# Kernel optimization log

Measured on AMD Instinct MI355X. Metric: run time of the kernel, lower is better.

## Reference

```python
import jax, jax.numpy as jnp
import numpy as np

# Dimensions (see shape_source)
N = 50000       # graph_size (number of nodes)
E_HALF = 300000 # undirected edges
E = 2 * E_HALF  # directed edges (both orientations)
D = 4           # stalk dimension d
H = 32          # hidden_channels


def _build_graph(seed=0):
    """Symmetric directed edge list: columns [0,E_HALF) are (u->v), columns
    [E_HALF, E) are the reversed (v->u). opp_idx[e] is the index of the
    opposite orientation of edge e (this is exactly the pairing computed by
    lap.compute_left_right_map_index in the torch module)."""
    rng = np.random.default_rng(seed)
    u = rng.integers(0, N, size=E_HALF)
    v = rng.integers(0, N, size=E_HALF)
    v = np.where(v == u, (v + 1) % N, v)  # no self-loops
    edge_index = np.stack([np.concatenate([u, v]), np.concatenate([v, u])]).astype(np.int32)
    opp = np.concatenate([np.arange(E_HALF) + E_HALF, np.arange(E_HALF)]).astype(np.int32)
    return jnp.asarray(edge_index), jnp.asarray(opp)


def setup_inputs() -> dict:
    key = jax.random.key(0)
    k1, k2, k3 = jax.random.split(key, 3)
    edge_index, opp_idx = _build_graph()
    x = jax.random.normal(k1, (N, D, H), dtype=jnp.float32)
    Maps = jax.random.normal(k2, (E, D, D), dtype=jnp.float32)
    # linear1: torch.nn.Linear(d*d, prod(out_shape)) with out_shape=(d,d)
    W1 = jax.random.normal(k3, (D * D, D * D), dtype=jnp.float32) / np.sqrt(D * D)
    b1 = jnp.zeros((D * D,), dtype=jnp.float32)
    return {"x": x, "Maps": Maps, "W1": W1, "b1": b1,
            "edge_index": edge_index, "opp_idx": opp_idx}


def reference(x, Maps, W1, b1, edge_index, opp_idx):
    # The dual-graph (nodes = directed edges) sheaf Laplacian of the
    # GeneralLaplacianBuilder reduces to a closed per-edge block form:
    # every dual node has degree 1, so deg-normalisation (deg_normalised=True,
    # augmented=False) is the identity. For directed edge e = (s -> t) with
    # opposite edge e' = opp_idx[e]:
    #   diag block of dual node e           =  X_s X_s^T
    #   off-diag block between e and e'     = -X_s X_t^T
    # spmm(L, Maps^T-blocks) followed by the x2 and transpose in forward gives
    #   sims_e = 2 * ( M_e (X_s X_s^T) - M_{e'} (X_t X_s^T) )
    s, t = edge_index[0], edge_index[1]
    Xs = x[s]                                   # (E, D, H) gather
    Xt = x[t]                                   # (E, D, H) gather
    G_ss = jnp.einsum('edh,ekh->edk', Xs, Xs)   # (E, D, D)  X_s X_s^T
    G_ts = jnp.einsum('edh,ekh->edk', Xt, Xs)   # (E, D, D)  X_t X_s^T
    sims = 2.0 * (jnp.einsum('eij,ejk->eik', Maps, G_ss)
                  - jnp.einsum('eij,ejk->eik', Maps[opp_idx], G_ts))
    # linear1 (torch Linear: y = x W^T + b) + tanh activation
    flat = sims.reshape(E, D * D) @ W1.T + b1
    return jnp.tanh(flat).reshape(E, D, D)      # out_shape = (d, d)
```

## Files before the change

kernel.cpp:

```cpp
#include <hip/hip_runtime.h>

constexpr int TPB = 256;
constexpr int PAIRS_PER_BLOCK = 32;

__device__ __forceinline__ float fast_tanh(float v) {
    float ex = __expf(2.0f * v);
    return 1.0f - 2.0f * __builtin_amdgcn_rcpf(ex + 1.0f);
}

template <int CTRL>
__device__ __forceinline__ float dppadd(float x) {
    return x + __int_as_float(__builtin_amdgcn_update_dpp(
        0, __float_as_int(x), CTRL, 0xf, 0xf, true));
}

__device__ __forceinline__ float sum8(float x) {
    x = dppadd<0x128>(x);
    x = dppadd<0x39>(x);
    x = dppadd<0x4E>(x);
    return x;
}

__global__ __launch_bounds__(TPB) void sheaf_p8_kernel(
    const float* __restrict__ x,
    const float* __restrict__ Maps,
    const float* __restrict__ W1,
    const float* __restrict__ b1,
    const int*   __restrict__ edge_index,
    const int*   __restrict__ opp_idx,
    float*       __restrict__ out,
    int E, int EHALF)
{
    const int tid    = threadIdx.x;
    const int lane16 = tid & 15;
    const int row16  = tid >> 4;
    const int pinr   = (lane16 >> 2) & 1;
    const int slot   = (lane16 & 3) | (((lane16 >> 3) & 1) << 2);
    const int pair   = blockIdx.x * PAIRS_PER_BLOCK + row16 * 2 + pinr;
    if (pair >= EHALF) return;

    const int s  = edge_index[pair];
    const int t  = edge_index[E + pair];
    const int e2 = opp_idx[pair];

    const float* xu = x + (size_t)s * 128 + slot * 4;
    const float* xv = x + (size_t)t * 128 + slot * 4;
    float4 u[4], v[4];
    #pragma unroll
    for (int d = 0; d < 4; ++d) {
        u[d] = *(const float4*)(xu + d * 32);
        v[d] = *(const float4*)(xv + d * 32);
    }

    const int p0 = 2 * slot;
    float wA[16], wB[16];
    {
        const float4* WpA = (const float4*)(W1 + p0 * 16);
        const float4* WpB = (const float4*)(W1 + (p0 + 1) * 16);
        #pragma unroll
        for (int q4 = 0; q4 < 4; ++q4) {
            float4 a = WpA[q4], b = WpB[q4];
            wA[q4*4+0] = a.x; wA[q4*4+1] = a.y; wA[q4*4+2] = a.z; wA[q4*4+3] = a.w;
            wB[q4*4+0] = b.x; wB[q4*4+1] = b.y; wB[q4*4+2] = b.z; wB[q4*4+3] = b.w;
        }
    }
    const float2 bb = *(const float2*)(b1 + p0);

    const float4* M1p = (const float4*)(Maps + (size_t)pair * 16);
    const float4* M2p = (const float4*)(Maps + (size_t)e2   * 16);

    float d1a = 0.f, d1b = 0.f, d2a = 0.f, d2b = 0.f;
    #pragma unroll
    for (int i = 0; i < 4; ++i) {
        const float4 m1 = M1p[i];
        const float4 m2 = M2p[i];
        float4 zi;
        zi.x = m1.x * u[0].x;            zi.y = m1.x * u[0].y;
        zi.z = m1.x * u[0].z;            zi.w = m1.x * u[0].w;
        zi.x = fmaf(m1.y, u[1].x, zi.x); zi.y = fmaf(m1.y, u[1].y, zi.y);
        zi.z = fmaf(m1.y, u[1].z, zi.z); zi.w = fmaf(m1.y, u[1].w, zi.w);
        zi.x = fmaf(m1.z, u[2].x, zi.x); zi.y = fmaf(m1.z, u[2].y, zi.y);
        zi.z = fmaf(m1.z, u[2].z, zi.z); zi.w = fmaf(m1.z, u[2].w, zi.w);
        zi.x = fmaf(m1.w, u[3].x, zi.x); zi.y = fmaf(m1.w, u[3].y, zi.y);
        zi.z = fmaf(m1.w, u[3].z, zi.z); zi.w = fmaf(m1.w, u[3].w, zi.w);
        zi.x = fmaf(-m2.x, v[0].x, zi.x); zi.y = fmaf(-m2.x, v[0].y, zi.y);
        zi.z = fmaf(-m2.x, v[0].z, zi.z); zi.w = fmaf(-m2.x, v[0].w, zi.w);
        zi.x = fmaf(-m2.y, v[1].x, zi.x); zi.y = fmaf(-m2.y, v[1].y, zi.y);
        zi.z = fmaf(-m2.y, v[1].z, zi.z); zi.w = fmaf(-m2.y, v[1].w, zi.w);
        zi.x = fmaf(-m2.z, v[2].x, zi.x); zi.y = fmaf(-m2.z, v[2].y, zi.y);
        zi.z = fmaf(-m2.z, v[2].z, zi.z); zi.w = fmaf(-m2.z, v[2].w, zi.w);
        zi.x = fmaf(-m2.w, v[3].x, zi.x); zi.y = fmaf(-m2.w, v[3].y, zi.y);
        zi.z = fmaf(-m2.w, v[3].z, zi.z); zi.w = fmaf(-m2.w, v[3].w, zi.w);

        #pragma unroll
        for (int k = 0; k < 4; ++k) {
            float pa = zi.x * u[k].x;
            pa = fmaf(zi.y, u[k].y, pa);
            pa = fmaf(zi.z, u[k].z, pa);
            pa = fmaf(zi.w, u[k].w, pa);
            float pb = zi.x * v[k].x;
            pb = fmaf(zi.y, v[k].y, pb);
            pb = fmaf(zi.z, v[k].z, pb);
            pb = fmaf(zi.w, v[k].w, pb);
            const float r1 = sum8(pa);
            const float r2 = sum8(pb);
            const int q = i * 4 + k;
            d1a = fmaf(wA[q], r1, d1a);
            d1b = fmaf(wB[q], r1, d1b);
            d2a = fmaf(wA[q], r2, d2a);
            d2b = fmaf(wB[q], r2, d2b);
        }
    }

    const float o1a = fast_tanh(fmaf( 2.0f, d1a, bb.x));
    const float o1b = fast_tanh(fmaf( 2.0f, d1b, bb.y));
    const float o2a = fast_tanh(fmaf(-2.0f, d2a, bb.x));
    const float o2b = fast_tanh(fmaf(-2.0f, d2b, bb.y));

    *(float2*)(out + (size_t)pair * 16 + p0) = make_float2(o1a, o1b);
    *(float2*)(out + (size_t)e2   * 16 + p0) = make_float2(o2a, o2b);
}

extern "C" void kernel_launch(void* const* d_in, const int* in_sizes, int n_in,
                              void* d_out, int out_size, void* d_ws, size_t ws_size,
                              hipStream_t stream) {
    const float* x          = (const float*)d_in[0];
    const float* Maps       = (const float*)d_in[1];
    const float* W1         = (const float*)d_in[2];
    const float* b1         = (const float*)d_in[3];
    const int*   edge_index = (const int*)d_in[4];
    const int*   opp_idx    = (const int*)d_in[5];

    const int E     = in_sizes[5];
    const int EHALF = E / 2;

    const int blocks = (EHALF + PAIRS_PER_BLOCK - 1) / PAIRS_PER_BLOCK;
    sheaf_p8_kernel<<<blocks, TPB, 0, stream>>>(
        x, Maps, W1, b1, edge_index, opp_idx, (float*)d_out, E, EHALF);
}
```

Before: 65.52 us.

## Convert to persistent grid-stride kernel with software-pipelined double-buffered loads

Replaces the one-chunk-per-block launch with a persistent grid of at most 1024 blocks that loop over pair chunks. Each iteration prefetches indices two chunks ahead and x/Maps data one chunk ahead into register double buffers while the current chunk is computed, so gather latency overlaps compute. W1 and bias are loaded once per thread and reused. The extra register buffers may cut occupancy, and fewer resident blocks reduce hardware latency hiding.

```diff
diff --git a/kernel.cpp b/kernel.cpp
--- a/kernel.cpp
+++ b/kernel.cpp
@@ -1,7 +1,7 @@
 #include <hip/hip_runtime.h>
 
 constexpr int TPB = 256;
-constexpr int PAIRS_PER_BLOCK = 32;
+constexpr int PPB = 32;
 
 __device__ __forceinline__ float fast_tanh(float v) {
     float ex = __expf(2.0f * v);
@@ -21,7 +21,7 @@
     return x;
 }
 
-__global__ __launch_bounds__(TPB) void sheaf_p8_kernel(
+__global__ __launch_bounds__(TPB) void sheaf_pipe_kernel(
     const float* __restrict__ x,
     const float* __restrict__ Maps,
     const float* __restrict__ W1,
@@ -36,21 +36,7 @@
     const int row16  = tid >> 4;
     const int pinr   = (lane16 >> 2) & 1;
     const int slot   = (lane16 & 3) | (((lane16 >> 3) & 1) << 2);
-    const int pair   = blockIdx.x * PAIRS_PER_BLOCK + row16 * 2 + pinr;
-    if (pair >= EHALF) return;
-
-    const int s  = edge_index[pair];
-    const int t  = edge_index[E + pair];
-    const int e2 = opp_idx[pair];
-
-    const float* xu = x + (size_t)s * 128 + slot * 4;
-    const float* xv = x + (size_t)t * 128 + slot * 4;
-    float4 u[4], v[4];
-    #pragma unroll
-    for (int d = 0; d < 4; ++d) {
-        u[d] = *(const float4*)(xu + d * 32);
-        v[d] = *(const float4*)(xv + d * 32);
-    }
+    const int NC     = (EHALF + PPB - 1) / PPB;
 
     const int p0 = 2 * slot;
     float wA[16], wB[16];
@@ -66,59 +52,124 @@
     }
     const float2 bb = *(const float2*)(b1 + p0);
 
-    const float4* M1p = (const float4*)(Maps + (size_t)pair * 16);
-    const float4* M2p = (const float4*)(Maps + (size_t)e2   * 16);
+    auto pairOf = [&](int c) { return c * PPB + row16 * 2 + pinr; };
 
-    float d1a = 0.f, d1b = 0.f, d2a = 0.f, d2b = 0.f;
-    #pragma unroll
-    for (int i = 0; i < 4; ++i) {
-        const float4 m1 = M1p[i];
-        const float4 m2 = M2p[i];
-        float4 zi;
-        zi.x = m1.x * u[0].x;            zi.y = m1.x * u[0].y;
-        zi.z = m1.x * u[0].z;            zi.w = m1.x * u[0].w;
-        zi.x = fmaf(m1.y, u[1].x, zi.x); zi.y = fmaf(m1.y, u[1].y, zi.y);
-        zi.z = fmaf(m1.y, u[1].z, zi.z); zi.w = fmaf(m1.y, u[1].w, zi.w);
-        zi.x = fmaf(m1.z, u[2].x, zi.x); zi.y = fmaf(m1.z, u[2].y, zi.y);
-        zi.z = fmaf(m1.z, u[2].z, zi.z); zi.w = fmaf(m1.z, u[2].w, zi.w);
-        zi.x = fmaf(m1.w, u[3].x, zi.x); zi.y = fmaf(m1.w, u[3].y, zi.y);
-        zi.z = fmaf(m1.w, u[3].z, zi.z); zi.w = fmaf(m1.w, u[3].w, zi.w);
-        zi.x = fmaf(-m2.x, v[0].x, zi.x); zi.y = fmaf(-m2.x, v[0].y, zi.y);
-        zi.z = fmaf(-m2.x, v[0].z, zi.z); zi.w = fmaf(-m2.x, v[0].w, zi.w);
-        zi.x = fmaf(-m2.y, v[1].x, zi.x); zi.y = fmaf(-m2.y, v[1].y, zi.y);
-        zi.z = fmaf(-m2.y, v[1].z, zi.z); zi.w = fmaf(-m2.y, v[1].w, zi.w);
-        zi.x = fmaf(-m2.z, v[2].x, zi.x); zi.y = fmaf(-m2.z, v[2].y, zi.y);
-        zi.z = fmaf(-m2.z, v[2].z, zi.z); zi.w = fmaf(-m2.z, v[2].w, zi.w);
-        zi.x = fmaf(-m2.w, v[3].x, zi.x); zi.y = fmaf(-m2.w, v[3].y, zi.y);
-        zi.z = fmaf(-m2.w, v[3].z, zi.z); zi.w = fmaf(-m2.w, v[3].w, zi.w);
+    auto loadIdx = [&](int c, int& s, int& t, int& e2) {
+        int pr = pairOf(c);
+        int pc = pr < EHALF ? pr : EHALF - 1;
+        s  = edge_index[pc];
+        t  = edge_index[E + pc];
+        e2 = opp_idx[pc];
+    };
+    auto loadX = [&](int s, int t, float4 (&u)[4], float4 (&v)[4]) {
+        const float* xu = x + (size_t)s * 128 + slot * 4;
+        const float* xv = x + (size_t)t * 128 + slot * 4;
+        #pragma unroll
+        for (int d = 0; d < 4; ++d) {
+            u[d] = *(const float4*)(xu + d * 32);
+            v[d] = *(const float4*)(xv + d * 32);
+        }
+    };
+    auto loadMaps = [&](int c, int e2, float4 (&m1)[4], float4 (&m2)[4]) {
+        int pr = pairOf(c);
+        int pc = pr < EHALF ? pr : EHALF - 1;
+        const float4* M1p = (const float4*)(Maps + (size_t)pc * 16);
+        const float4* M2p = (const float4*)(Maps + (size_t)e2 * 16);
+        #pragma unroll
+        for (int i = 0; i < 4; ++i) { m1[i] = M1p[i]; m2[i] = M2p[i]; }
+    };
 
+    auto computeStore = [&](int c, int e2,
+                            const float4 (&u)[4], const float4 (&v)[4],
+                            const float4 (&m1)[4], const float4 (&m2)[4]) {
+        float d1a = 0.f, d1b = 0.f, d2a = 0.f, d2b = 0.f;
         #pragma unroll
-        for (int k = 0; k < 4; ++k) {
-            float pa = zi.x * u[k].x;
-            pa = fmaf(zi.y, u[k].y, pa);
-            pa = fmaf(zi.z, u[k].z, pa);
-            pa = fmaf(zi.w, u[k].w, pa);
-            float pb = zi.x * v[k].x;
-            pb = fmaf(zi.y, v[k].y, pb);
-            pb = fmaf(zi.z, v[k].z, pb);
-            pb = fmaf(zi.w, v[k].w, pb);
-            const float r1 = sum8(pa);
-            const float r2 = sum8(pb);
-            const int q = i * 4 + k;
-            d1a = fmaf(wA[q], r1, d1a);
-            d1b = fmaf(wB[q], r1, d1b);
-            d2a = fmaf(wA[q], r2, d2a);
-            d2b = fmaf(wB[q], r2, d2b);
+        for (int i = 0; i < 4; ++i) {
+            const float4 M1 = m1[i], M2 = m2[i];
+            float4 zi;
+            zi.x = M1.x * u[0].x;            zi.y = M1.x * u[0].y;
+            zi.z = M1.x * u[0].z;            zi.w = M1.x * u[0].w;
+            zi.x = fmaf(M1.y, u[1].x, zi.x); zi.y = fmaf(M1.y, u[1].y, zi.y);
+            zi.z = fmaf(M1.y, u[1].z, zi.z); zi.w = fmaf(M1.y, u[1].w, zi.w);
+            zi.x = fmaf(M1.z, u[2].x, zi.x); zi.y = fmaf(M1.z, u[2].y, zi.y);
+            zi.z = fmaf(M1.z, u[2].z, zi.z); zi.w = fmaf(M1.z, u[2].w, zi.w);
+            zi.x = fmaf(M1.w, u[3].x, zi.x); zi.y = fmaf(M1.w, u[3].y, zi.y);
+            zi.z = fmaf(M1.w, u[3].z, zi.z); zi.w = fmaf(M1.w, u[3].w, zi.w);
+            zi.x = fmaf(-M2.x, v[0].x, zi.x); zi.y = fmaf(-M2.x, v[0].y, zi.y);
+            zi.z = fmaf(-M2.x, v[0].z, zi.z); zi.w = fmaf(-M2.x, v[0].w, zi.w);
+            zi.x = fmaf(-M2.y, v[1].x, zi.x); zi.y = fmaf(-M2.y, v[1].y, zi.y);
+            zi.z = fmaf(-M2.y, v[1].z, zi.z); zi.w = fmaf(-M2.y, v[1].w, zi.w);
+            zi.x = fmaf(-M2.z, v[2].x, zi.x); zi.y = fmaf(-M2.z, v[2].y, zi.y);
+            zi.z = fmaf(-M2.z, v[2].z, zi.z); zi.w = fmaf(-M2.z, v[2].w, zi.w);
+            zi.x = fmaf(-M2.w, v[3].x, zi.x); zi.y = fmaf(-M2.w, v[3].y, zi.y);
+            zi.z = fmaf(-M2.w, v[3].z, zi.z); zi.w = fmaf(-M2.w, v[3].w, zi.w);
+
+            #pragma unroll
+            for (int k = 0; k < 4; ++k) {
+                float pa = zi.x * u[k].x;
+                pa = fmaf(zi.y, u[k].y, pa);
+                pa = fmaf(zi.z, u[k].z, pa);
+                pa = fmaf(zi.w, u[k].w, pa);
+                float pb = zi.x * v[k].x;
+                pb = fmaf(zi.y, v[k].y, pb);
+                pb = fmaf(zi.z, v[k].z, pb);
+                pb = fmaf(zi.w, v[k].w, pb);
+                const float r1 = sum8(pa);
+                const float r2 = sum8(pb);
+                const int q = i * 4 + k;
+                d1a = fmaf(wA[q], r1, d1a);
+                d1b = fmaf(wB[q], r1, d1b);
+                d2a = fmaf(wA[q], r2, d2a);
+                d2b = fmaf(wB[q], r2, d2b);
+            }
         }
+        const float o1a = fast_tanh(fmaf( 2.0f, d1a, bb.x));
+        const float o1b = fast_tanh(fmaf( 2.0f, d1b, bb.y));
+        const float o2a = fast_tanh(fmaf(-2.0f, d2a, bb.x));
+        const float o2b = fast_tanh(fmaf(-2.0f, d2b, bb.y));
+
+        const int pr = pairOf(c);
+        if (pr < EHALF) {
+            *(float2*)(out + (size_t)pr * 16 + p0) = make_float2(o1a, o1b);
+            *(float2*)(out + (size_t)e2 * 16 + p0) = make_float2(o2a, o2b);
+        }
+    };
+
+    const int G = gridDim.x;
+    int cC = blockIdx.x;
+    if (cC >= NC) return;
+
+    float4 u0[4], v0[4], m10[4], m20[4];
+    float4 u1[4], v1[4], m11[4], m21[4];
+    int s1 = 0, t1 = 0, e1 = 0;
+    int sp = 0, tp = 0, ep = 0;
+
+    int s0, t0, e0;
+    loadIdx(cC, s0, t0, e0);
+    loadX(s0, t0, u0, v0);
+    loadMaps(cC, e0, m10, m20);
+    int cL = cC + G;
+    if (cL < NC) loadIdx(cL, s1, t1, e1);
+
+    for (;;) {
+        int cP = cL + G;
+        if (cL < NC) { loadX(s1, t1, u1, v1); loadMaps(cL, e1, m11, m21); }
+        if (cP < NC) loadIdx(cP, sp, tp, ep);
+        computeStore(cC, e0, u0, v0, m10, m20);
+        if (cL >= NC) return;
+        cC = cL; cL = cP;
+
+        int cP2 = cL + G;
+        if (cL < NC) { loadX(sp, tp, u0, v0); loadMaps(cL, ep, m10, m20); }
+        int sq = 0, tq = 0, eq = 0;
+        if (cP2 < NC) loadIdx(cP2, sq, tq, eq);
+        computeStore(cC, e1, u1, v1, m11, m21);
+        if (cL >= NC) return;
+        cC = cL; cL = cP2;
+
+        e0 = ep;
+        s1 = sq; t1 = tq; e1 = eq;
     }
-
-    const float o1a = fast_tanh(fmaf( 2.0f, d1a, bb.x));
-    const float o1b = fast_tanh(fmaf( 2.0f, d1b, bb.y));
-    const float o2a = fast_tanh(fmaf(-2.0f, d2a, bb.x));
-    const float o2b = fast_tanh(fmaf(-2.0f, d2b, bb.y));
-
-    *(float2*)(out + (size_t)pair * 16 + p0) = make_float2(o1a, o1b);
-    *(float2*)(out + (size_t)e2   * 16 + p0) = make_float2(o2a, o2b);
 }
 
 extern "C" void kernel_launch(void* const* d_in, const int* in_sizes, int n_in,
@@ -133,8 +184,9 @@
 
     const int E     = in_sizes[5];
     const int EHALF = E / 2;
+    const int NC    = (EHALF + PPB - 1) / PPB;
 
-    const int blocks = (EHALF + PAIRS_PER_BLOCK - 1) / PAIRS_PER_BLOCK;
-    sheaf_p8_kernel<<<blocks, TPB, 0, stream>>>(
+    const int blocks = NC < 1024 ? NC : 1024;
+    sheaf_pipe_kernel<<<blocks, TPB, 0, stream>>>(
         x, Maps, W1, b1, edge_index, opp_idx, (float*)d_out, E, EHALF);
 }
```

Result: faster. 60.71 us (-7.3%).
